# Kernel optimization log

Measured on AMD Instinct MI355X. Metric: run time of the kernel, lower is better.

Reference implementation:

```python
import jax, jax.numpy as jnp
import numpy as np

S_DIM, I_DIM, O_DIM = 1024, 2048, 1024
TOTAL = S_DIM + I_DIM + O_DIM  # 4096
INPUT_DIM, NUM_CLASSES, BATCH = 2048, 1000, 256


def setup_inputs() -> dict:
    key = jax.random.key(0)
    ks = jax.random.split(key, 6)
    x = jax.random.normal(ks[0], (BATCH, INPUT_DIM), dtype=jnp.float32)
    W = jax.random.normal(ks[1], (TOTAL, TOTAL), dtype=jnp.float32) * 0.02
    # torch Linear: weight [out, in], bias [out]
    in_w = jax.random.normal(ks[2], (S_DIM, INPUT_DIM), dtype=jnp.float32) * (1.0 / np.sqrt(INPUT_DIM))
    in_b = jax.random.normal(ks[3], (S_DIM,), dtype=jnp.float32) * 0.01
    out_w = jax.random.normal(ks[4], (NUM_CLASSES, O_DIM), dtype=jnp.float32) * (1.0 / np.sqrt(O_DIM))
    out_b = jax.random.normal(ks[5], (NUM_CLASSES,), dtype=jnp.float32) * 0.01
    return {"x": x, "W": W, "in_w": in_w, "in_b": in_b, "out_w": out_w, "out_b": out_b, "time_steps": 10}


def reference(x, W, in_w, in_b, out_w, out_b, time_steps):
    B = x.shape[0]
    S, I, O = S_DIM, I_DIM, O_DIM
    # slice effective W into 9 sub-blocks (use_lora=False -> W_eff = W)
    W_ss, W_sr, W_so = W[:S, :S], W[:S, S:S + I], W[:S, S + I:]
    W_rs, W_rr, W_ro = W[S:S + I, :S], W[S:S + I, S:S + I], W[S:S + I, S + I:]
    W_os, W_or, W_oo = W[S + I:, :S], W[S + I:, S:S + I], W[S + I:, S + I:]

    E = x @ in_w.T + in_b  # [B, S]
    gate = (jnp.arange(time_steps) % 5 == 0).astype(x.dtype)  # E injected when t%5==0

    init = (jnp.zeros((B, S), x.dtype), jnp.zeros((B, I), x.dtype), jnp.zeros((B, O), x.dtype))

    def step(carry, g):
        Ss, Is, Os = carry
        S_next = jax.nn.relu(Ss @ W_ss + g * E + Is @ W_rs + Os @ W_os)
        I_next = jax.nn.relu(Is @ W_rr + Ss @ W_sr + Os @ W_or)
        O_next = jax.nn.relu(Os @ W_oo + Is @ W_ro + Ss @ W_so)
        return (S_next, I_next, O_next), None

    (Ss, Is, Os), _ = jax.lax.scan(step, init, gate)
    return Os @ out_w.T + out_b  # [B, num_classes]
```

## Files before the change

### kernel.cpp

```cpp
#include <hip/hip_runtime.h>


typedef __bf16 bf16x8 __attribute__((ext_vector_type(8)));
typedef float  f32x16 __attribute__((ext_vector_type(16)));

#define TOTAL 4096
#define BATCH 256
#define INDIM 2048
#define SDIM  1024
#define NCLS  1000

#define MFMA(a, b, c) __builtin_amdgcn_mfma_f32_32x32x16_bf16((a), (b), (c), 0, 0, 0)

__device__ inline f32x16 zero16() {
    f32x16 v;
#pragma unroll
    for (int i = 0; i < 16; ++i) v[i] = 0.f;
    return v;
}

__device__ inline void swz_slot(const float* __restrict__ in, __bf16* __restrict__ out,
                                int C, int Rvalid, int t) {
    const int lane = t & 63;
    const int frag = t >> 6;
    const int kcN = C >> 4;
    const int rt = frag / kcN;
    const int kc = frag - rt * kcN;
    const int r = rt * 32 + (lane & 31);
    const int c = kc * 16 + (lane >> 5) * 8;
    alignas(16) __bf16 v[8];
    if (r < Rvalid) {
        const float* p = in + (size_t)r * C + c;
#pragma unroll
        for (int j = 0; j < 8; ++j) v[j] = (__bf16)p[j];
    } else {
#pragma unroll
        for (int j = 0; j < 8; ++j) v[j] = (__bf16)0.f;
    }
    *(ulonglong2*)(out + (size_t)t * 8) = *(const ulonglong2*)v;
}

__global__ __launch_bounds__(256) void k_prep(const float* __restrict__ W,
                                              const float* __restrict__ x,
                                              const float* __restrict__ in_w,
                                              const float* __restrict__ in_b,
                                              const float* __restrict__ out_w,
                                              __bf16* __restrict__ WT,
                                              __bf16* __restrict__ OWT,
                                              float* __restrict__ Ebuf,
                                              __bf16* __restrict__ H0) {
    __shared__ float t[64][65];
    const int bid = blockIdx.x;
    const int tid = threadIdx.x;
    if (bid < 4096) {
        const int n0 = (bid & 63) * 64;
        const int k0 = (bid >> 6) * 64;
        const int rr = tid >> 4;
        const int cc = (tid & 15) * 4;
#pragma unroll
        for (int p = 0; p < 4; ++p) {
            const int r = p * 16 + rr;
            float4 v = *(const float4*)(W + (size_t)(k0 + r) * TOTAL + n0 + cc);
            t[r][cc] = v.x; t[r][cc + 1] = v.y; t[r][cc + 2] = v.z; t[r][cc + 3] = v.w;
        }
        __syncthreads();
#pragma unroll
        for (int s = tid; s < 512; s += 256) {
            const int frag = s >> 6;
            const int lane = s & 63;
            const int lrt = frag >> 2;
            const int lkc = frag & 3;
            const int r_local = lrt * 32 + (lane & 31);
            const int c_local = lkc * 16 + (lane >> 5) * 8;
            alignas(16) __bf16 v[8];
#pragma unroll
            for (int j = 0; j < 8; ++j) v[j] = (__bf16)t[c_local + j][r_local];
            const size_t fragG = (size_t)((n0 >> 5) + lrt) * (TOTAL / 16) + ((k0 >> 4) + lkc);
            *(ulonglong2*)(WT + fragG * 512 + lane * 8) = *(const ulonglong2*)v;
        }
    } else if (bid < 4352) {
        float* red = &t[0][0];
        const int eb = bid - 4096;
        const int mt = eb >> 5, nt = eb & 31;
        const int wave = tid >> 6, lane = tid & 63;
        const int l31 = lane & 31, kh = (lane >> 5) * 8;
        const int k0 = wave * 512;
        const float* Ax = x    + (size_t)(mt * 32 + l31) * INDIM + k0 + kh;
        const float* Bw = in_w + (size_t)(nt * 32 + l31) * INDIM + k0 + kh;
        f32x16 acc = zero16();
#pragma unroll 4
        for (int i = 0; i < 32; ++i) {
            const float* pa = Ax + i * 16;
            const float* pb = Bw + i * 16;
            float4 a0 = *(const float4*)pa, a1 = *(const float4*)(pa + 4);
            float4 b0 = *(const float4*)pb, b1 = *(const float4*)(pb + 4);
            bf16x8 a, b;
            a[0] = (__bf16)a0.x; a[1] = (__bf16)a0.y; a[2] = (__bf16)a0.z; a[3] = (__bf16)a0.w;
            a[4] = (__bf16)a1.x; a[5] = (__bf16)a1.y; a[6] = (__bf16)a1.z; a[7] = (__bf16)a1.w;
            b[0] = (__bf16)b0.x; b[1] = (__bf16)b0.y; b[2] = (__bf16)b0.z; b[3] = (__bf16)b0.w;
            b[4] = (__bf16)b1.x; b[5] = (__bf16)b1.y; b[6] = (__bf16)b1.z; b[7] = (__bf16)b1.w;
            acc = MFMA(a, b, acc);
        }
#pragma unroll
        for (int r = 0; r < 16; ++r) {
            int row = (r & 3) + 8 * (r >> 2) + 4 * (lane >> 5);
            red[wave * 1024 + row * 32 + l31] = acc[r];
        }
        __syncthreads();
        const int e0 = tid * 4;
        float4 s = {0.f, 0.f, 0.f, 0.f};
#pragma unroll
        for (int w = 0; w < 4; ++w) {
            float4 v = *(const float4*)&red[w * 1024 + e0];
            s.x += v.x; s.y += v.y; s.z += v.z; s.w += v.w;
        }
        const int row = e0 >> 5, col = e0 & 31;
        const int m = mt * 32 + row, n = nt * 32 + col;
        float v[4] = {s.x + in_b[n], s.y + in_b[n + 1], s.z + in_b[n + 2], s.w + in_b[n + 3]};
        *(float4*)(Ebuf + m * SDIM + n) = *(const float4*)v;
        alignas(8) __bf16 o[4];
#pragma unroll
        for (int j = 0; j < 4; ++j) o[j] = (__bf16)fmaxf(v[j], 0.f);
        const size_t frag = (size_t)(m >> 5) * (TOTAL / 16) + (n >> 4);
        const int lh = (m & 31) + 32 * ((n >> 3) & 1);
        *(ushort4*)(H0 + frag * 512 + lh * 8 + (n & 7)) = *(const ushort4*)o;
    } else {
        swz_slot(out_w, OWT, 1024, NCLS, (bid - 4352) * 256 + tid);
    }
}

template <int CHUNKS>
__global__ __launch_bounds__(512, 2) void k_step(const __bf16* __restrict__ h,
                                                 const __bf16* __restrict__ WT,
                                                 const float* __restrict__ E,
                                                 const int gate,
                                                 __bf16* __restrict__ hn) {
    __shared__ float buf[4][4096];
    const int wave = threadIdx.x >> 6;
    const int lane = threadIdx.x & 63;
    const int mt = blockIdx.x >> 6;
    const int nt = blockIdx.x & 63;
    constexpr int PER = CHUNKS >> 3;
    const int kc0 = wave * PER;

    const bf16x8* A0 = (const bf16x8*)h  + ((size_t)(mt * 2) * (TOTAL / 16) + kc0) * 64 + lane;
    const bf16x8* A1 = A0 + (size_t)(TOTAL / 16) * 64;
    const bf16x8* B0 = (const bf16x8*)WT + ((size_t)(nt * 2) * (TOTAL / 16) + kc0) * 64 + lane;
    const bf16x8* B1 = B0 + (size_t)(TOTAL / 16) * 64;

    f32x16 ac0 = zero16(), ac1 = zero16(), ac2 = zero16(), ac3 = zero16();
#pragma unroll 4
    for (int i = 0; i < PER; ++i) {
        const int off = i * 64;
        bf16x8 a0 = A0[off];
        bf16x8 a1 = A1[off];
        bf16x8 b0 = B0[off];
        bf16x8 b1 = B1[off];
        ac0 = MFMA(a0, b0, ac0);
        ac1 = MFMA(a0, b1, ac1);
        ac2 = MFMA(a1, b0, ac2);
        ac3 = MFMA(a1, b1, ac3);
    }

    f32x16 accs[4] = {ac0, ac1, ac2, ac3};
    if (wave >= 4) {
        float* b = buf[wave - 4];
#pragma unroll
        for (int c = 0; c < 4; ++c)
#pragma unroll
            for (int r = 0; r < 16; ++r)
                b[(c * 16 + r) * 64 + lane] = accs[c][r];
    }
    __syncthreads();
    if (wave < 4) {
        float* b = buf[wave];
#pragma unroll
        for (int c = 0; c < 4; ++c)
#pragma unroll
            for (int r = 0; r < 16; ++r) {
                const int idx = (c * 16 + r) * 64 + lane;
                b[idx] += accs[c][r];
            }
    }
    __syncthreads();

    const int t = threadIdx.x;
    const int c = t >> 7;
    const int r = (t >> 3) & 15;
    const int l0 = (t & 7) * 8;
    const int base = (c * 16 + r) * 64 + l0;
    float4 s0 = {0.f, 0.f, 0.f, 0.f}, s1 = {0.f, 0.f, 0.f, 0.f};
#pragma unroll
    for (int w = 0; w < 4; ++w) {
        const float4* p = (const float4*)&buf[w][base];
        float4 v0 = p[0], v1 = p[1];
        s0.x += v0.x; s0.y += v0.y; s0.z += v0.z; s0.w += v0.w;
        s1.x += v1.x; s1.y += v1.y; s1.z += v1.z; s1.w += v1.w;
    }
    float v[8] = {s0.x, s0.y, s0.z, s0.w, s1.x, s1.y, s1.z, s1.w};
    const int ih = c >> 1, jh = c & 1;
    const int row = ih * 32 + (r & 3) + 8 * (r >> 2) + 4 * (l0 >> 5);
    const int col0 = jh * 32 + (l0 & 31);
    const int m = mt * 64 + row;
    const int n0g = nt * 64 + col0;
    if (gate && n0g < SDIM) {
        const float* Ep = E + m * SDIM + n0g;
#pragma unroll
        for (int j = 0; j < 8; ++j) v[j] += Ep[j];
    }
    alignas(16) __bf16 o[8];
#pragma unroll
    for (int j = 0; j < 8; ++j) o[j] = (__bf16)fmaxf(v[j], 0.f);
    const size_t frag = (size_t)(m >> 5) * (TOTAL / 16) + (n0g >> 4);
    const int lh = (m & 31) + 32 * ((n0g >> 3) & 1);
    *(ulonglong2*)(hn + frag * 512 + lh * 8) = *(const ulonglong2*)o;
}

__global__ __launch_bounds__(512, 4) void k_out(const __bf16* __restrict__ h,
                                                const __bf16* __restrict__ owt,
                                                const float* __restrict__ out_b,
                                                float* __restrict__ out) {
    __shared__ float red[8][1024];
    const int wave = threadIdx.x >> 6;
    const int lane = threadIdx.x & 63;
    const int mt = blockIdx.x >> 5;
    const int ct = blockIdx.x & 31;
    const int m0 = mt * 32, c0 = ct * 32;
    const int kcA0 = (3072 / 16) + wave * 8;
    const int kcB0 = wave * 8;
    const bf16x8* Ap = (const bf16x8*)h   + ((size_t)mt * (TOTAL / 16) + kcA0) * 64 + lane;
    const bf16x8* Bp = (const bf16x8*)owt + ((size_t)ct * (1024 / 16) + kcB0) * 64 + lane;
    f32x16 acc = zero16();
#pragma unroll
    for (int i = 0; i < 8; ++i)
        acc = MFMA(Ap[i * 64], Bp[i * 64], acc);
#pragma unroll
    for (int r = 0; r < 16; ++r) {
        int row = (r & 3) + 8 * (r >> 2) + 4 * (lane >> 5);
        red[wave][row * 32 + (lane & 31)] = acc[r];
    }
    __syncthreads();
    const int e0 = threadIdx.x * 2;
    float sx = 0.f, sy = 0.f;
#pragma unroll
    for (int w = 0; w < 8; ++w) {
        float2 v = *(const float2*)&red[w][e0];
        sx += v.x; sy += v.y;
    }
    const int row = e0 >> 5, col = e0 & 31;
    const int m = m0 + row;
    const int n = c0 + col;
    if (n < NCLS)     out[m * NCLS + n]     = sx + out_b[n];
    if (n + 1 < NCLS) out[m * NCLS + n + 1] = sy + out_b[n + 1];
}

extern "C" void kernel_launch(void* const* d_in, const int* in_sizes, int n_in,
                              void* d_out, int out_size, void* d_ws, size_t ws_size,
                              hipStream_t stream) {
    const float* x     = (const float*)d_in[0];
    const float* W     = (const float*)d_in[1];
    const float* in_w  = (const float*)d_in[2];
    const float* in_b  = (const float*)d_in[3];
    const float* out_w = (const float*)d_in[4];
    const float* out_b = (const float*)d_in[5];
    float* out = (float*)d_out;

    char* ws = (char*)d_ws;
    __bf16* WT  = (__bf16*)(ws + 0);
    __bf16* OWT = (__bf16*)(ws + 33554432);
    float*  Ebuf= (float*)(ws + 35651584);
    __bf16* H0  = (__bf16*)(ws + 36700160);
    __bf16* H1  = (__bf16*)(ws + 38797312);

    k_prep<<<4864, 256, 0, stream>>>(W, x, in_w, in_b, out_w, WT, OWT, Ebuf, H0);

    const __bf16* hs = H0;
    __bf16* hd = H1;
    for (int t = 1; t < 10; ++t) {
        const int gate = (t % 5 == 0) ? 1 : 0;
        if (t == 1)
            k_step<SDIM / 16><<<256, 512, 0, stream>>>(hs, WT, Ebuf, gate, hd);
        else
            k_step<TOTAL / 16><<<256, 512, 0, stream>>>(hs, WT, Ebuf, gate, hd);
        const __bf16* tmp = hs; hs = hd; hd = (__bf16*)tmp;
    }

    k_out<<<256, 512, 0, stream>>>(hs, OWT, out_b, out);
}
```

Before: 296.8 us.

## Reorder prep blocks, vectorize W transpose reads, and remap step blocks per XCD

The prep kernel now schedules the E-projection blocks first and the W transpose blocks after them. The transpose stores into shared memory already transposed, so each lane reads 8 contiguous floats with two float4 loads instead of eight strided scalar reads. The step kernel's block-index mapping is changed so that blocks landing on the same XCD share the same column tiles of WT across all four row tiles. The aim is better L2 reuse of weights per XCD, with scattered shared-memory writes as the trade-off.

Result: faster. 266.4 us (-10.2%).

```diff
diff --git a/kernel.cpp b/kernel.cpp
--- a/kernel.cpp
+++ b/kernel.cpp
@@ -52,36 +52,9 @@
     __shared__ float t[64][65];
     const int bid = blockIdx.x;
     const int tid = threadIdx.x;
-    if (bid < 4096) {
-        const int n0 = (bid & 63) * 64;
-        const int k0 = (bid >> 6) * 64;
-        const int rr = tid >> 4;
-        const int cc = (tid & 15) * 4;
-#pragma unroll
-        for (int p = 0; p < 4; ++p) {
-            const int r = p * 16 + rr;
-            float4 v = *(const float4*)(W + (size_t)(k0 + r) * TOTAL + n0 + cc);
-            t[r][cc] = v.x; t[r][cc + 1] = v.y; t[r][cc + 2] = v.z; t[r][cc + 3] = v.w;
-        }
-        __syncthreads();
-#pragma unroll
-        for (int s = tid; s < 512; s += 256) {
-            const int frag = s >> 6;
-            const int lane = s & 63;
-            const int lrt = frag >> 2;
-            const int lkc = frag & 3;
-            const int r_local = lrt * 32 + (lane & 31);
-            const int c_local = lkc * 16 + (lane >> 5) * 8;
-            alignas(16) __bf16 v[8];
-#pragma unroll
-            for (int j = 0; j < 8; ++j) v[j] = (__bf16)t[c_local + j][r_local];
-            const size_t fragG = (size_t)((n0 >> 5) + lrt) * (TOTAL / 16) + ((k0 >> 4) + lkc);
-            *(ulonglong2*)(WT + fragG * 512 + lane * 8) = *(const ulonglong2*)v;
-        }
-    } else if (bid < 4352) {
+    if (bid < 256) {
         float* red = &t[0][0];
-        const int eb = bid - 4096;
-        const int mt = eb >> 5, nt = eb & 31;
+        const int mt = bid >> 5, nt = bid & 31;
         const int wave = tid >> 6, lane = tid & 63;
         const int l31 = lane & 31, kh = (lane >> 5) * 8;
         const int k0 = wave * 512;
@@ -124,6 +97,35 @@
         const size_t frag = (size_t)(m >> 5) * (TOTAL / 16) + (n >> 4);
         const int lh = (m & 31) + 32 * ((n >> 3) & 1);
         *(ushort4*)(H0 + frag * 512 + lh * 8 + (n & 7)) = *(const ushort4*)o;
+    } else if (bid < 4352) {
+        const int wb = bid - 256;
+        const int n0 = (wb & 63) * 64;
+        const int k0 = (wb >> 6) * 64;
+        const int rr = tid >> 4;
+        const int cc = (tid & 15) * 4;
+#pragma unroll
+        for (int p = 0; p < 4; ++p) {
+            const int k = p * 16 + rr;
+            float4 v = *(const float4*)(W + (size_t)(k0 + k) * TOTAL + n0 + cc);
+            t[cc][k] = v.x; t[cc + 1][k] = v.y; t[cc + 2][k] = v.z; t[cc + 3][k] = v.w;
+        }
+        __syncthreads();
+#pragma unroll
+        for (int s = tid; s < 512; s += 256) {
+            const int frag = s >> 6;
+            const int lane = s & 63;
+            const int lrt = frag >> 2;
+            const int lkc = frag & 3;
+            const int nl = lrt * 32 + (lane & 31);
+            const int kl = lkc * 16 + (lane >> 5) * 8;
+            float4 f0 = *(const float4*)&t[nl][kl];
+            float4 f1 = *(const float4*)&t[nl][kl + 4];
+            bf16x8 v;
+            v[0] = (__bf16)f0.x; v[1] = (__bf16)f0.y; v[2] = (__bf16)f0.z; v[3] = (__bf16)f0.w;
+            v[4] = (__bf16)f1.x; v[5] = (__bf16)f1.y; v[6] = (__bf16)f1.z; v[7] = (__bf16)f1.w;
+            const size_t fragG = (size_t)((n0 >> 5) + lrt) * (TOTAL / 16) + ((k0 >> 4) + lkc);
+            *(bf16x8*)(WT + fragG * 512 + lane * 8) = v;
+        }
     } else {
         swz_slot(out_w, OWT, 1024, NCLS, (bid - 4352) * 256 + tid);
     }
@@ -138,8 +140,10 @@
     __shared__ float buf[4][4096];
     const int wave = threadIdx.x >> 6;
     const int lane = threadIdx.x & 63;
-    const int mt = blockIdx.x >> 6;
-    const int nt = blockIdx.x & 63;
+    const int xcd = blockIdx.x & 7;
+    const int idx = blockIdx.x >> 3;
+    const int mt = idx & 3;
+    const int nt = xcd * 8 + (idx >> 2);
     constexpr int PER = CHUNKS >> 3;
     const int kc0 = wave * PER;
 
@@ -178,8 +182,8 @@
         for (int c = 0; c < 4; ++c)
 #pragma unroll
             for (int r = 0; r < 16; ++r) {
-                const int idx = (c * 16 + r) * 64 + lane;
-                b[idx] += accs[c][r];
+                const int i2 = (c * 16 + r) * 64 + lane;
+                b[i2] += accs[c][r];
             }
     }
     __syncthreads();
```
